# Kernel optimization log

Measured on AMD Instinct MI355X. Metric: run time of the kernel, lower is better.

Reference implementation:

```python
import jax, jax.numpy as jnp
import numpy as np

N_NODES = 100000
N_GRAPHS = 512


def gcn_conv(x, W, b, src, dst, n):
    # PyG GCNConv: h = x @ W; add self-loops; sym-normalize; scatter-add to dst; + bias
    h = x @ W
    loop = jnp.arange(n, dtype=src.dtype)
    s = jnp.concatenate([src, loop])
    d = jnp.concatenate([dst, loop])
    deg = jax.ops.segment_sum(jnp.ones_like(d, dtype=h.dtype), d, num_segments=n)
    dinv = jnp.where(deg > 0, jax.lax.rsqrt(deg), 0.0)
    norm = dinv[s] * dinv[d]               # [E+N]
    msg = h[s] * norm[:, None]             # gather + scale
    out = jax.ops.segment_sum(msg, d, num_segments=n)
    return out + b


def setup_inputs() -> dict:
    key = jax.random.key(0)
    ks = jax.random.split(key, 12)
    F_in, H, C = 128, 128, 10
    x = jax.random.normal(ks[0], (N_NODES, F_in), dtype=jnp.float32)
    edge_index = jax.random.randint(ks[1], (2, 3200000), 0, N_NODES, dtype=jnp.int64)
    batch = jnp.sort(jax.random.randint(ks[2], (N_NODES,), 0, N_GRAPHS, dtype=jnp.int64))
    def glorot(k, fi, fo):
        s = jnp.sqrt(6.0 / (fi + fo))
        return jax.random.uniform(k, (fi, fo), dtype=jnp.float32, minval=-s, maxval=s)
    return {
        "x": x, "edge_index": edge_index, "batch": batch,
        "W_in": glorot(ks[3], F_in, H), "b_in": jnp.zeros((H,), jnp.float32),
        "W_h0": glorot(ks[4], H, H), "b_h0": jnp.zeros((H,), jnp.float32),
        "W_h1": glorot(ks[5], H, H), "b_h1": jnp.zeros((H,), jnp.float32),
        "W_out": glorot(ks[6], H, C), "b_out": jnp.zeros((C,), jnp.float32),
    }


def reference(x, edge_index, batch, W_in, b_in, W_h0, b_h0, W_h1, b_h1, W_out, b_out):
    src, dst = edge_index[0], edge_index[1]
    n = x.shape[0]
    h = jax.nn.relu(gcn_conv(x, W_in, b_in, src, dst, n))
    h = jax.nn.relu(gcn_conv(h, W_h0, b_h0, src, dst, n))
    h = jax.nn.relu(gcn_conv(h, W_h1, b_h1, src, dst, n))
    h = gcn_conv(h, W_out, b_out, src, dst, n)
    # global_mean_pool over graph ids
    sums = jax.ops.segment_sum(h, batch, num_segments=N_GRAPHS)
    cnts = jax.ops.segment_sum(jnp.ones((n,), h.dtype), batch, num_segments=N_GRAPHS)
    pooled = sums / jnp.maximum(cnts, 1.0)[:, None]
    return jax.nn.log_softmax(pooled, axis=-1)
```

## Files before the change

kernel.cpp:

```cpp
#include <hip/hip_runtime.h>
#include <math.h>

#define TPB 256
#define MAXDEG 80
#define SHIFT 8
#define BNODES 256
#define CAP 10240
#define EPB 4096
#define LSTR 136

typedef short bf16x8 __attribute__((ext_vector_type(8)));
typedef float f32x4 __attribute__((ext_vector_type(4)));

__device__ inline unsigned short f2bf(float f) {
    unsigned u = __float_as_uint(f);
    return (unsigned short)((u + 0x7fffu + ((u >> 16) & 1u)) >> 16);
}
__device__ inline float bflo(unsigned u) { return __uint_as_float(u << 16); }
__device__ inline float bfhi(unsigned u) { return __uint_as_float(u & 0xffff0000u); }


__global__ __launch_bounds__(TPB) void p1_k(const int* __restrict__ src,
                                            const int* __restrict__ dst,
                                            int* __restrict__ gbcnt,
                                            int* __restrict__ buckets, int E, int nb) {
    __shared__ int hist[512];
    __shared__ int lcur[512];
    int tid = threadIdx.x;
    for (int b = tid; b < nb; b += TPB) hist[b] = 0;
    __syncthreads();
    int e0 = blockIdx.x * EPB;
    int m = E - e0; if (m > EPB) m = EPB;
    for (int i = tid; i < m; i += TPB)
        atomicAdd(&hist[dst[e0 + i] >> SHIFT], 1);
    __syncthreads();
    for (int b = tid; b < nb; b += TPB) {
        int h = hist[b];
        lcur[b] = h ? atomicAdd(&gbcnt[b], h) : 0;
    }
    __syncthreads();
    for (int i = tid; i < m; i += TPB) {
        int d = dst[e0 + i];
        int s = src[e0 + i];
        int b = d >> SHIFT;
        int pos = atomicAdd(&lcur[b], 1);
        if (pos < CAP) buckets[(size_t)b * CAP + pos] = (s << SHIFT) | (d & (BNODES - 1));
    }
}


__global__ __launch_bounds__(TPB) void p2_k(const int* __restrict__ gbcnt,
                                            const int* __restrict__ buckets,
                                            int* __restrict__ csr,
                                            int* __restrict__ deg,
                                            float* __restrict__ dinv, int n) {
    __shared__ int lcnt[BNODES];
    int b = blockIdx.x, tid = threadIdx.x;
    lcnt[tid] = 0;
    __syncthreads();
    int m = gbcnt[b]; if (m > CAP) m = CAP;
    const int* bp = buckets + (size_t)b * CAP;
    int vb = b << SHIFT;
    for (int i = tid; i < m; i += TPB) {
        int rec = bp[i];
        int dl = rec & (BNODES - 1);
        int pos = atomicAdd(&lcnt[dl], 1);
        if (pos < MAXDEG) csr[(size_t)(vb + dl) * MAXDEG + pos] = rec >> SHIFT;
    }
    __syncthreads();
    int v = vb + tid;
    if (v < n) {
        int c = lcnt[tid];
        deg[v] = c < MAXDEG ? c : MAXDEG;
        dinv[v] = rsqrtf((float)(c + 1));
    }
}


__global__ __launch_bounds__(TPB) void wcast_k(const float* __restrict__ W0,
                                               const float* __restrict__ W1,
                                               const float* __restrict__ W2,
                                               unsigned short* __restrict__ T0,
                                               unsigned short* __restrict__ T1,
                                               unsigned short* __restrict__ T2) {
    const float* W = blockIdx.x == 0 ? W0 : (blockIdx.x == 1 ? W1 : W2);
    unsigned short* T = blockIdx.x == 0 ? T0 : (blockIdx.x == 1 ? T1 : T2);
    for (int idx = threadIdx.x; idx < 16384; idx += TPB) {
        int nn = idx >> 7, kk = idx & 127;
        T[idx] = f2bf(W[kk * 128 + nn]);
    }
}


__device__ __forceinline__ void mfma_tile(const unsigned short* Hs,
                                          const unsigned short* __restrict__ WT,
                                          const float* __restrict__ dinv,
                                          unsigned short* __restrict__ gout,
                                          int vb, int n, int w, int l) {
    f32x4 acc[2][8];
#pragma unroll
    for (int a = 0; a < 2; a++)
#pragma unroll
        for (int b = 0; b < 8; b++)
#pragma unroll
            for (int j = 0; j < 4; j++) acc[a][b][j] = 0.f;
    const int quad = l >> 4, lm = l & 15;
    const int mrow0 = w * 32;
#pragma unroll
    for (int ks = 0; ks < 4; ks++) {
        bf16x8 a0 = *(const bf16x8*)(Hs + (mrow0 + lm) * LSTR + ks * 32 + quad * 8);
        bf16x8 a1 = *(const bf16x8*)(Hs + (mrow0 + 16 + lm) * LSTR + ks * 32 + quad * 8);
#pragma unroll
        for (int nt = 0; nt < 8; nt++) {
            bf16x8 bf = *(const bf16x8*)(WT + (size_t)(nt * 16 + lm) * 128 + ks * 32 + quad * 8);
            acc[0][nt] = __builtin_amdgcn_mfma_f32_16x16x32_bf16(a0, bf, acc[0][nt], 0, 0, 0);
            acc[1][nt] = __builtin_amdgcn_mfma_f32_16x16x32_bf16(a1, bf, acc[1][nt], 0, 0, 0);
        }
    }
#pragma unroll
    for (int mt = 0; mt < 2; mt++) {
#pragma unroll
        for (int j = 0; j < 4; j++) {
            int r = vb + mrow0 + mt * 16 + quad * 4 + j;
            if (r < n) {
                float s = dinv[r];
#pragma unroll
                for (int nt = 0; nt < 8; nt++)
                    gout[(size_t)r * 128 + nt * 16 + lm] = f2bf(acc[mt][nt][j] * s);
            }
        }
    }
}


__global__ __launch_bounds__(256) void gemm_f32in(const float* __restrict__ x,
                                                  const unsigned short* __restrict__ WT,
                                                  const float* __restrict__ dinv,
                                                  unsigned short* __restrict__ gout, int n) {
    __shared__ unsigned short Hs[128 * LSTR];
    int tid = threadIdx.x;
    int vb = blockIdx.x * 128;
    for (int i = tid; i < 8192; i += 256) {
        int row = i >> 6, cw = i & 63;
        int gr = vb + row; if (gr > n - 1) gr = n - 1;
        float2 xv = *(const float2*)(x + (size_t)gr * 128 + cw * 2);
        unsigned pk = ((unsigned)f2bf(xv.y) << 16) | f2bf(xv.x);
        *(unsigned*)(Hs + row * LSTR + cw * 2) = pk;
    }
    __syncthreads();
    mfma_tile(Hs, WT, dinv, gout, vb, n, tid >> 6, tid & 63);
}


__global__ __launch_bounds__(256) void gemm_bf16in(const unsigned* __restrict__ hin,
                                                   const unsigned short* __restrict__ WT,
                                                   const float* __restrict__ dinv,
                                                   unsigned short* __restrict__ gout, int n) {
    __shared__ unsigned short Hs[128 * LSTR];
    int tid = threadIdx.x;
    int vb = blockIdx.x * 128;
    for (int i = tid; i < 8192; i += 256) {
        int row = i >> 6, cw = i & 63;
        int gr = vb + row; if (gr > n - 1) gr = n - 1;
        *(unsigned*)(Hs + row * LSTR + cw * 2) = hin[(size_t)gr * 64 + cw];
    }
    __syncthreads();
    mfma_tile(Hs, WT, dinv, gout, vb, n, tid >> 6, tid & 63);
}


__global__ __launch_bounds__(256) void aggb_k(const unsigned* __restrict__ g,
                                              const float* __restrict__ dinv,
                                              const int* __restrict__ deg,
                                              const int* __restrict__ csr,
                                              const float* __restrict__ bias,
                                              unsigned* __restrict__ hout, int n) {
    int w = __builtin_amdgcn_readfirstlane((int)(threadIdx.x >> 6));
    int l = threadIdx.x & 63;
    int v = blockIdx.x * 4 + w;
    if (v >= n) return;
    unsigned u = g[(size_t)v * 64 + l];
    float acc0 = bflo(u), acc1 = bfhi(u);
    const int* cp = csr + (size_t)v * MAXDEG;
    int d = deg[v];
    int e = 0;
    for (; e + 8 <= d; e += 8) {
        int s0 = cp[e], s1 = cp[e + 1], s2 = cp[e + 2], s3 = cp[e + 3];
        int s4 = cp[e + 4], s5 = cp[e + 5], s6 = cp[e + 6], s7 = cp[e + 7];
        unsigned u0 = g[(size_t)s0 * 64 + l];
        unsigned u1 = g[(size_t)s1 * 64 + l];
        unsigned u2 = g[(size_t)s2 * 64 + l];
        unsigned u3 = g[(size_t)s3 * 64 + l];
        unsigned u4 = g[(size_t)s4 * 64 + l];
        unsigned u5 = g[(size_t)s5 * 64 + l];
        unsigned u6 = g[(size_t)s6 * 64 + l];
        unsigned u7 = g[(size_t)s7 * 64 + l];
        acc0 += (bflo(u0) + bflo(u1)) + (bflo(u2) + bflo(u3))
              + (bflo(u4) + bflo(u5)) + (bflo(u6) + bflo(u7));
        acc1 += (bfhi(u0) + bfhi(u1)) + (bfhi(u2) + bfhi(u3))
              + (bfhi(u4) + bfhi(u5)) + (bfhi(u6) + bfhi(u7));
    }
    for (; e < d; e++) {
        unsigned ux = g[(size_t)cp[e] * 64 + l];
        acc0 += bflo(ux); acc1 += bfhi(ux);
    }
    float2 bb = *(const float2*)(bias + 2 * l);
    float s = dinv[v];
    float o0 = fmaxf(s * acc0 + bb.x, 0.f);
    float o1 = fmaxf(s * acc1 + bb.y, 0.f);
    hout[(size_t)v * 64 + l] = ((unsigned)f2bf(o1) << 16) | f2bf(o0);
}


__global__ __launch_bounds__(256) void fused_thin(const unsigned* __restrict__ gin,
                                                  const float* __restrict__ Wout,
                                                  const float* __restrict__ dinv,
                                                  const int* __restrict__ deg,
                                                  const int* __restrict__ csr,
                                                  const float* __restrict__ bias,
                                                  float* __restrict__ g4, int n) {
    __shared__ float Wl[1280];
    int tid = threadIdx.x;
    for (int i = tid; i < 1280; i += 256) Wl[i] = Wout[i];
    __syncthreads();
    int w = __builtin_amdgcn_readfirstlane((int)(tid >> 6));
    int l = tid & 63;
    int v = blockIdx.x * 4 + w;
    if (v >= n) return;
    unsigned u = gin[(size_t)v * 64 + l];
    float acc0 = bflo(u), acc1 = bfhi(u);
    const int* cp = csr + (size_t)v * MAXDEG;
    int d = deg[v];
    int e = 0;
    for (; e + 8 <= d; e += 8) {
        int s0 = cp[e], s1 = cp[e + 1], s2 = cp[e + 2], s3 = cp[e + 3];
        int s4 = cp[e + 4], s5 = cp[e + 5], s6 = cp[e + 6], s7 = cp[e + 7];
        unsigned u0 = gin[(size_t)s0 * 64 + l];
        unsigned u1 = gin[(size_t)s1 * 64 + l];
        unsigned u2 = gin[(size_t)s2 * 64 + l];
        unsigned u3 = gin[(size_t)s3 * 64 + l];
        unsigned u4 = gin[(size_t)s4 * 64 + l];
        unsigned u5 = gin[(size_t)s5 * 64 + l];
        unsigned u6 = gin[(size_t)s6 * 64 + l];
        unsigned u7 = gin[(size_t)s7 * 64 + l];
        acc0 += (bflo(u0) + bflo(u1)) + (bflo(u2) + bflo(u3))
              + (bflo(u4) + bflo(u5)) + (bflo(u6) + bflo(u7));
        acc1 += (bfhi(u0) + bfhi(u1)) + (bfhi(u2) + bfhi(u3))
              + (bfhi(u4) + bfhi(u5)) + (bfhi(u6) + bfhi(u7));
    }
    for (; e < d; e++) {
        unsigned ux = gin[(size_t)cp[e] * 64 + l];
        acc0 += bflo(ux); acc1 += bfhi(ux);
    }
    float2 bb = *(const float2*)(bias + 2 * l);
    float s = dinv[v];
    float o0 = fmaxf(s * acc0 + bb.x, 0.f);
    float o1 = fmaxf(s * acc1 + bb.y, 0.f);
    float p[10];
#pragma unroll
    for (int c = 0; c < 10; c++)
        p[c] = o0 * Wl[(2 * l) * 10 + c] + o1 * Wl[(2 * l + 1) * 10 + c];
#pragma unroll
    for (int off = 32; off; off >>= 1)
#pragma unroll
        for (int c = 0; c < 10; c++) p[c] += __shfl_down(p[c], off, 64);
    if (l == 0) {
#pragma unroll
        for (int c = 0; c < 10; c++) g4[(size_t)v * 10 + c] = s * p[c];
    }
}


__global__ __launch_bounds__(TPB) void agg_thin(const float* __restrict__ g,
                                                const float* __restrict__ dinv,
                                                const int* __restrict__ deg,
                                                const int* __restrict__ csr,
                                                const float* __restrict__ bias,
                                                float* __restrict__ out, int n) {
    int idx = blockIdx.x * TPB + threadIdx.x;
    if (idx >= n * 10) return;
    int v = idx / 10, c = idx - v * 10;
    float acc = g[(size_t)v * 10 + c];
    size_t s0 = (size_t)v * MAXDEG;
    int d = deg[v];
    for (int e = 0; e < d; e++) acc += g[(size_t)csr[s0 + e] * 10 + c];
    out[idx] = dinv[v] * acc + bias[c];
}


#define POOL_SPAN 8

__global__ __launch_bounds__(TPB) void pool_k(const float* __restrict__ h,
                                              const int* __restrict__ batch,
                                              float* __restrict__ pool, int* __restrict__ cnt, int n) {
    __shared__ float lp[POOL_SPAN][10];
    __shared__ int lc[POOL_SPAN];
    __shared__ int g0;
    int tid = threadIdx.x;
    int v = blockIdx.x * TPB + tid;
    if (tid == 0) {
        int first = blockIdx.x * TPB;
        if (first > n - 1) first = n - 1;
        g0 = batch[first];
    }
    if (tid < POOL_SPAN) lc[tid] = 0;
    if (tid < POOL_SPAN * 10) lp[tid / 10][tid % 10] = 0.f;
    __syncthreads();
    if (v < n) {
        int gi = batch[v];
        int o = gi - g0;
        if (o < POOL_SPAN) {
            atomicAdd(&lc[o], 1);
#pragma unroll
            for (int c = 0; c < 10; c++) atomicAdd(&lp[o][c], h[(size_t)v * 10 + c]);
        } else {
            atomicAdd(&cnt[gi], 1);
#pragma unroll
            for (int c = 0; c < 10; c++) atomicAdd(&pool[gi * 10 + c], h[(size_t)v * 10 + c]);
        }
    }
    __syncthreads();
    if (tid < POOL_SPAN) {
        if (lc[tid] > 0) atomicAdd(&cnt[g0 + tid], lc[tid]);
    }
    if (tid < POOL_SPAN * 10) {
        int o = tid / 10, c = tid % 10;
        if (lc[o] > 0) atomicAdd(&pool[(g0 + o) * 10 + c], lp[o][c]);
    }
}

__global__ __launch_bounds__(TPB) void final_k(const float* __restrict__ pool,
                                               const int* __restrict__ cnt,
                                               float* __restrict__ out, int ng) {
    int gi = blockIdx.x * TPB + threadIdx.x;
    if (gi >= ng) return;
    float cn = fmaxf((float)cnt[gi], 1.f);
    float x[10];
    float m = -1e30f;
#pragma unroll
    for (int c = 0; c < 10; c++) {
        x[c] = pool[gi * 10 + c] / cn;
        m = fmaxf(m, x[c]);
    }
    float s = 0.f;
#pragma unroll
    for (int c = 0; c < 10; c++) s += expf(x[c] - m);
    float l = logf(s);
#pragma unroll
    for (int c = 0; c < 10; c++) out[gi * 10 + c] = x[c] - m - l;
}


extern "C" void kernel_launch(void* const* d_in, const int* in_sizes, int n_in,
                              void* d_out, int out_size, void* d_ws, size_t ws_size,
                              hipStream_t stream) {
    const float* x    = (const float*)d_in[0];
    const int*   ei   = (const int*)d_in[1];
    const int*   batch= (const int*)d_in[2];
    const float* W_in = (const float*)d_in[3];
    const float* b_in = (const float*)d_in[4];
    const float* W_h0 = (const float*)d_in[5];
    const float* b_h0 = (const float*)d_in[6];
    const float* W_h1 = (const float*)d_in[7];
    const float* b_h1 = (const float*)d_in[8];
    const float* W_out= (const float*)d_in[9];
    const float* b_out= (const float*)d_in[10];

    const int n  = in_sizes[2];
    const int E  = in_sizes[1] / 2;
    const int ng = out_size / 10;
    const int nb = (n + BNODES - 1) >> SHIFT;

    char* p = (char*)d_ws;
    auto carve = [&](size_t bytes) { void* r = (void*)p; p += (bytes + 255) & ~(size_t)255; return r; };
    int*            deg    = (int*)           carve((size_t)n * 4);
    float*          dinv   = (float*)         carve((size_t)n * 4);
    int*            gbcnt  = (int*)           carve((size_t)nb * 4);
    int*            buckets= (int*)           carve((size_t)nb * CAP * 4);
    int*            csr    = (int*)           carve((size_t)n * MAXDEG * 4);
    unsigned*       G      = (unsigned*)      carve((size_t)n * 64 * 4);
    unsigned*       H      = (unsigned*)      carve((size_t)n * 64 * 4);
    unsigned short* WT0    = (unsigned short*)carve(16384 * 2);
    unsigned short* WT1    = (unsigned short*)carve(16384 * 2);
    unsigned short* WT2    = (unsigned short*)carve(16384 * 2);
    float*          g10    = (float*)         carve((size_t)n * 10 * 4);
    float*          h10    = (float*)         carve((size_t)n * 10 * 4);
    float*          pool   = (float*)         carve((size_t)ng * 10 * 4);
    int*            cnt    = (int*)           carve((size_t)ng * 4);

    (void)hipMemsetAsync(gbcnt, 0, (size_t)nb * 4, stream);
    (void)hipMemsetAsync(pool, 0, (size_t)ng * 10 * 4, stream);
    (void)hipMemsetAsync(cnt, 0, (size_t)ng * 4, stream);

    const int gN = (n + TPB - 1) / TPB;
    const int gP1 = (E + EPB - 1) / EPB;
    const int gG = (n + 127) / 128;
    const int gA4 = (n + 3) / 4;

    p1_k<<<gP1, TPB, 0, stream>>>(ei, ei + E, gbcnt, buckets, E, nb);
    p2_k<<<nb, TPB, 0, stream>>>(gbcnt, buckets, csr, deg, dinv, n);
    wcast_k<<<3, TPB, 0, stream>>>(W_in, W_h0, W_h1, WT0, WT1, WT2);

    gemm_f32in<<<gG, 256, 0, stream>>>(x, WT0, dinv, (unsigned short*)G, n);
    aggb_k<<<gA4, 256, 0, stream>>>(G, dinv, deg, csr, b_in, H, n);
    gemm_bf16in<<<gG, 256, 0, stream>>>(H, WT1, dinv, (unsigned short*)G, n);
    aggb_k<<<gA4, 256, 0, stream>>>(G, dinv, deg, csr, b_h0, H, n);
    gemm_bf16in<<<gG, 256, 0, stream>>>(H, WT2, dinv, (unsigned short*)G, n);
    fused_thin<<<gA4, 256, 0, stream>>>(G, W_out, dinv, deg, csr, b_h1, g10, n);
    agg_thin<<<(n * 10 + TPB - 1) / TPB, TPB, 0, stream>>>(g10, dinv, deg, csr, b_out, h10, n);
    pool_k<<<gN, TPB, 0, stream>>>(h10, batch, pool, cnt, n);
    final_k<<<(ng + TPB - 1) / TPB, TPB, 0, stream>>>(pool, cnt, (float*)d_out, ng);
}
```

Before: 727.6 us.

## Sort CSR neighbors by source chunk and move output projection to MFMA

The CSR build now counts each destination's neighbors per source-index chunk, prefix-sums those counts and scatters the neighbors into chunk order. Neighbor lists are therefore roughly sorted by source, which should improve cache locality in the gather kernels. The fused layer-3 aggregate plus 128x10 projection, which used scalar dot products and wave shuffles, is replaced by the regular aggb_k followed by a new bf16 MFMA thin GEMM with the weight padded to 16 columns. This adds an extra kernel and a round trip of H through memory, and rounds the layer-3 output to bf16 before the projection.

Measured after the change: 707.0 us. -2.8%, faster.

```diff
diff --git a/kernel.cpp b/kernel.cpp
--- a/kernel.cpp
+++ b/kernel.cpp
@@ -8,6 +8,7 @@
 #define CAP 10240
 #define EPB 4096
 #define LSTR 136
+#define NCHUNK 13
 
 typedef short bf16x8 __attribute__((ext_vector_type(8)));
 typedef float f32x4 __attribute__((ext_vector_type(4)));
@@ -54,25 +55,35 @@
                                             int* __restrict__ csr,
                                             int* __restrict__ deg,
                                             float* __restrict__ dinv, int n) {
-    __shared__ int lcnt[BNODES];
+    __shared__ int cnt[BNODES][NCHUNK];
     int b = blockIdx.x, tid = threadIdx.x;
-    lcnt[tid] = 0;
+    for (int i = tid; i < BNODES * NCHUNK; i += TPB) ((int*)cnt)[i] = 0;
     __syncthreads();
     int m = gbcnt[b]; if (m > CAP) m = CAP;
     const int* bp = buckets + (size_t)b * CAP;
     int vb = b << SHIFT;
     for (int i = tid; i < m; i += TPB) {
         int rec = bp[i];
+        atomicAdd(&cnt[rec & (BNODES - 1)][(rec >> SHIFT) >> 13], 1);
+    }
+    __syncthreads();
+    {
+        int run = 0;
+#pragma unroll
+        for (int c = 0; c < NCHUNK; c++) { int t = cnt[tid][c]; cnt[tid][c] = run; run += t; }
+        int v = vb + tid;
+        if (v < n) {
+            deg[v] = run < MAXDEG ? run : MAXDEG;
+            dinv[v] = rsqrtf((float)(run + 1));
+        }
+    }
+    __syncthreads();
+    for (int i = tid; i < m; i += TPB) {
+        int rec = bp[i];
         int dl = rec & (BNODES - 1);
-        int pos = atomicAdd(&lcnt[dl], 1);
-        if (pos < MAXDEG) csr[(size_t)(vb + dl) * MAXDEG + pos] = rec >> SHIFT;
-    }
-    __syncthreads();
-    int v = vb + tid;
-    if (v < n) {
-        int c = lcnt[tid];
-        deg[v] = c < MAXDEG ? c : MAXDEG;
-        dinv[v] = rsqrtf((float)(c + 1));
+        int s = rec >> SHIFT;
+        int pos = atomicAdd(&cnt[dl][s >> 13], 1);
+        if (pos < MAXDEG) csr[(size_t)(vb + dl) * MAXDEG + pos] = s;
     }
 }
 
@@ -80,14 +91,24 @@
 __global__ __launch_bounds__(TPB) void wcast_k(const float* __restrict__ W0,
                                                const float* __restrict__ W1,
                                                const float* __restrict__ W2,
+                                               const float* __restrict__ W3,
                                                unsigned short* __restrict__ T0,
                                                unsigned short* __restrict__ T1,
-                                               unsigned short* __restrict__ T2) {
-    const float* W = blockIdx.x == 0 ? W0 : (blockIdx.x == 1 ? W1 : W2);
-    unsigned short* T = blockIdx.x == 0 ? T0 : (blockIdx.x == 1 ? T1 : T2);
-    for (int idx = threadIdx.x; idx < 16384; idx += TPB) {
-        int nn = idx >> 7, kk = idx & 127;
-        T[idx] = f2bf(W[kk * 128 + nn]);
+                                               unsigned short* __restrict__ T2,
+                                               unsigned short* __restrict__ T3) {
+    int b = blockIdx.x;
+    if (b < 3) {
+        const float* W = b == 0 ? W0 : (b == 1 ? W1 : W2);
+        unsigned short* T = b == 0 ? T0 : (b == 1 ? T1 : T2);
+        for (int idx = threadIdx.x; idx < 16384; idx += TPB) {
+            int nn = idx >> 7, kk = idx & 127;
+            T[idx] = f2bf(W[kk * 128 + nn]);
+        }
+    } else {
+        for (int idx = threadIdx.x; idx < 2048; idx += TPB) {
+            int nn = idx >> 7, kk = idx & 127;
+            T3[idx] = nn < 10 ? f2bf(W3[kk * 10 + nn]) : (unsigned short)0;
+        }
     }
 }
 
@@ -166,6 +187,47 @@
     }
     __syncthreads();
     mfma_tile(Hs, WT, dinv, gout, vb, n, tid >> 6, tid & 63);
+}
+
+
+__global__ __launch_bounds__(256) void thin_mfma(const unsigned* __restrict__ hin,
+                                                 const unsigned short* __restrict__ WT3,
+                                                 const float* __restrict__ dinv,
+                                                 float* __restrict__ g4, int n) {
+    __shared__ unsigned short Hs[128 * LSTR];
+    int tid = threadIdx.x;
+    int vb = blockIdx.x * 128;
+    for (int i = tid; i < 8192; i += 256) {
+        int row = i >> 6, cw = i & 63;
+        int gr = vb + row; if (gr > n - 1) gr = n - 1;
+        *(unsigned*)(Hs + row * LSTR + cw * 2) = hin[(size_t)gr * 64 + cw];
+    }
+    __syncthreads();
+    int w = tid >> 6, l = tid & 63;
+    int quad = l >> 4, lm = l & 15;
+    int mrow0 = w * 32;
+    f32x4 acc[2];
+#pragma unroll
+    for (int a = 0; a < 2; a++)
+#pragma unroll
+        for (int j = 0; j < 4; j++) acc[a][j] = 0.f;
+#pragma unroll
+    for (int ks = 0; ks < 4; ks++) {
+        bf16x8 a0 = *(const bf16x8*)(Hs + (mrow0 + lm) * LSTR + ks * 32 + quad * 8);
+        bf16x8 a1 = *(const bf16x8*)(Hs + (mrow0 + 16 + lm) * LSTR + ks * 32 + quad * 8);
+        bf16x8 bf = *(const bf16x8*)(WT3 + (size_t)lm * 128 + ks * 32 + quad * 8);
+        acc[0] = __builtin_amdgcn_mfma_f32_16x16x32_bf16(a0, bf, acc[0], 0, 0, 0);
+        acc[1] = __builtin_amdgcn_mfma_f32_16x16x32_bf16(a1, bf, acc[1], 0, 0, 0);
+    }
+    if (lm < 10) {
+#pragma unroll
+        for (int mt = 0; mt < 2; mt++)
+#pragma unroll
+            for (int j = 0; j < 4; j++) {
+                int r = vb + mrow0 + mt * 16 + quad * 4 + j;
+                if (r < n) g4[(size_t)r * 10 + lm] = dinv[r] * acc[mt][j];
+            }
+    }
 }
 
 
@@ -212,65 +274,6 @@
 }
 
 
-__global__ __launch_bounds__(256) void fused_thin(const unsigned* __restrict__ gin,
-                                                  const float* __restrict__ Wout,
-                                                  const float* __restrict__ dinv,
-                                                  const int* __restrict__ deg,
-                                                  const int* __restrict__ csr,
-                                                  const float* __restrict__ bias,
-                                                  float* __restrict__ g4, int n) {
-    __shared__ float Wl[1280];
-    int tid = threadIdx.x;
-    for (int i = tid; i < 1280; i += 256) Wl[i] = Wout[i];
-    __syncthreads();
-    int w = __builtin_amdgcn_readfirstlane((int)(tid >> 6));
-    int l = tid & 63;
-    int v = blockIdx.x * 4 + w;
-    if (v >= n) return;
-    unsigned u = gin[(size_t)v * 64 + l];
-    float acc0 = bflo(u), acc1 = bfhi(u);
-    const int* cp = csr + (size_t)v * MAXDEG;
-    int d = deg[v];
-    int e = 0;
-    for (; e + 8 <= d; e += 8) {
-        int s0 = cp[e], s1 = cp[e + 1], s2 = cp[e + 2], s3 = cp[e + 3];
-        int s4 = cp[e + 4], s5 = cp[e + 5], s6 = cp[e + 6], s7 = cp[e + 7];
-        unsigned u0 = gin[(size_t)s0 * 64 + l];
-        unsigned u1 = gin[(size_t)s1 * 64 + l];
-        unsigned u2 = gin[(size_t)s2 * 64 + l];
-        unsigned u3 = gin[(size_t)s3 * 64 + l];
-        unsigned u4 = gin[(size_t)s4 * 64 + l];
-        unsigned u5 = gin[(size_t)s5 * 64 + l];
-        unsigned u6 = gin[(size_t)s6 * 64 + l];
-        unsigned u7 = gin[(size_t)s7 * 64 + l];
-        acc0 += (bflo(u0) + bflo(u1)) + (bflo(u2) + bflo(u3))
-              + (bflo(u4) + bflo(u5)) + (bflo(u6) + bflo(u7));
-        acc1 += (bfhi(u0) + bfhi(u1)) + (bfhi(u2) + bfhi(u3))
-              + (bfhi(u4) + bfhi(u5)) + (bfhi(u6) + bfhi(u7));
-    }
-    for (; e < d; e++) {
-        unsigned ux = gin[(size_t)cp[e] * 64 + l];
-        acc0 += bflo(ux); acc1 += bfhi(ux);
-    }
-    float2 bb = *(const float2*)(bias + 2 * l);
-    float s = dinv[v];
-    float o0 = fmaxf(s * acc0 + bb.x, 0.f);
-    float o1 = fmaxf(s * acc1 + bb.y, 0.f);
-    float p[10];
-#pragma unroll
-    for (int c = 0; c < 10; c++)
-        p[c] = o0 * Wl[(2 * l) * 10 + c] + o1 * Wl[(2 * l + 1) * 10 + c];
-#pragma unroll
-    for (int off = 32; off; off >>= 1)
-#pragma unroll
-        for (int c = 0; c < 10; c++) p[c] += __shfl_down(p[c], off, 64);
-    if (l == 0) {
-#pragma unroll
-        for (int c = 0; c < 10; c++) g4[(size_t)v * 10 + c] = s * p[c];
-    }
-}
-
-
 __global__ __launch_bounds__(TPB) void agg_thin(const float* __restrict__ g,
                                                 const float* __restrict__ dinv,
                                                 const int* __restrict__ deg,
@@ -383,6 +386,7 @@
     unsigned short* WT0    = (unsigned short*)carve(16384 * 2);
     unsigned short* WT1    = (unsigned short*)carve(16384 * 2);
     unsigned short* WT2    = (unsigned short*)carve(16384 * 2);
+    unsigned short* WT3    = (unsigned short*)carve(2048 * 2);
     float*          g10    = (float*)         carve((size_t)n * 10 * 4);
     float*          h10    = (float*)         carve((size_t)n * 10 * 4);
     float*          pool   = (float*)         carve((size_t)ng * 10 * 4);
@@ -399,14 +403,15 @@
 
     p1_k<<<gP1, TPB, 0, stream>>>(ei, ei + E, gbcnt, buckets, E, nb);
     p2_k<<<nb, TPB, 0, stream>>>(gbcnt, buckets, csr, deg, dinv, n);
-    wcast_k<<<3, TPB, 0, stream>>>(W_in, W_h0, W_h1, WT0, WT1, WT2);
+    wcast_k<<<4, TPB, 0, stream>>>(W_in, W_h0, W_h1, W_out, WT0, WT1, WT2, WT3);
 
     gemm_f32in<<<gG, 256, 0, stream>>>(x, WT0, dinv, (unsigned short*)G, n);
     aggb_k<<<gA4, 256, 0, stream>>>(G, dinv, deg, csr, b_in, H, n);
     gemm_bf16in<<<gG, 256, 0, stream>>>(H, WT1, dinv, (unsigned short*)G, n);
     aggb_k<<<gA4, 256, 0, stream>>>(G, dinv, deg, csr, b_h0, H, n);
     gemm_bf16in<<<gG, 256, 0, stream>>>(H, WT2, dinv, (unsigned short*)G, n);
-    fused_thin<<<gA4, 256, 0, stream>>>(G, W_out, dinv, deg, csr, b_h1, g10, n);
+    aggb_k<<<gA4, 256, 0, stream>>>(G, dinv, deg, csr, b_h1, H, n);
+    thin_mfma<<<gG, 256, 0, stream>>>(H, WT3, dinv, g10, n);
     agg_thin<<<(n * 10 + TPB - 1) / TPB, TPB, 0, stream>>>(g10, dinv, deg, csr, b_out, h10, n);
     pool_k<<<gN, TPB, 0, stream>>>(h10, batch, pool, cnt, n);
     final_k<<<(ng + TPB - 1) / TPB, TPB, 0, stream>>>(pool, cnt, (float*)d_out, ng);
```
